# Kernel tuning notes

Hardware: AMD Instinct MI355X
Metric: run time of the kernel (lower is better)

Reference implementation:

```python
import jax, jax.numpy as jnp
import numpy as np

PI = float(np.pi)


def _cgs(node_feats, node_centre, nbr_idx, graph_w,
         mean_rho, mean_theta, prec_rho, prec_theta, conv_w, use_graph_weights):
    # node_feats: [B,N,C]; node_centre: [B,N,2]; nbr_idx: [B,N,K] (within-sample node ids)
    # graph_w: [B*N*K, 1] or None; mean/prec: [1,R]; conv_w: [R, C, OUT//R]
    B, N, C = node_feats.shape
    K = nbr_idx.shape[-1]
    R = mean_rho.shape[-1]
    BN = B * N
    # flat neighbor index into B*N nodes (coords[1])
    flat_nbr = (jnp.arange(B, dtype=nbr_idx.dtype)[:, None, None] * N + nbr_idx).reshape(BN * K)
    src = jnp.repeat(jnp.arange(BN), K)
    centre = node_centre.reshape(BN, 2)
    d = centre[src] - centre[flat_nbr]                    # [E,2], node_intersect 'minus'
    rho = jnp.sqrt(d[:, 0] ** 2 + d[:, 1] ** 2)
    theta = jnp.arctan2(d[:, 0], d[:, 1])
    # gaussian mixture edge weights over R kernels
    w_rho = jnp.exp(-0.5 * (rho[:, None] - mean_rho) ** 2 / (1e-14 + prec_rho ** 2))
    first_angle = jnp.abs(theta[:, None] - mean_theta)
    second_angle = jnp.abs(2.0 * PI - first_angle)
    w_theta = jnp.exp(-0.5 * jnp.minimum(first_angle, second_angle) ** 2
                      / (1e-14 + prec_theta ** 2))
    w = w_rho * w_theta
    w = jnp.where(jnp.isnan(w), 0.0, w)
    w = w / jnp.sum(w, axis=1, keepdims=True)             # [E,R]
    if use_graph_weights:
        w = graph_w * w
    ew = w.reshape(BN, K, R)
    nj = node_feats.reshape(BN, C)[flat_nbr].reshape(BN, K, C)   # gather neighbors
    agg = jnp.einsum('ekr,ekc->erc', ew, nj).reshape(B, N, R, C)  # weighted bmm
    out = jnp.einsum('bnrc,rcd->bnrd', agg, conv_w).reshape(B, N, R * conv_w.shape[-1])
    return jax.nn.relu(out)


def setup_inputs() -> dict:
    key = jax.random.key(0)
    ks = jax.random.split(key, 16)
    B, N, K, C, R, OUT = 64, 100, 16, 1024, 8, 1024
    D = OUT // R
    return {
        "node_feats": jax.random.normal(ks[0], (B, N, C), jnp.float32),
        "node_centre": jax.random.uniform(ks[1], (B, N, 2), dtype=jnp.float32),
        "graph_w": jax.random.uniform(ks[2], (B * N * K, 1), dtype=jnp.float32),
        "nbr_idx": jax.random.randint(ks[3], (B, N, K), 0, N, dtype=jnp.int32),
        "mean_rho1": jax.random.uniform(ks[4], (1, R), dtype=jnp.float32),
        "mean_theta1": jax.random.uniform(ks[5], (1, R), dtype=jnp.float32, minval=-PI, maxval=PI),
        "prec_rho1": jax.random.uniform(ks[6], (1, R), dtype=jnp.float32),
        "prec_theta1": jax.random.uniform(ks[7], (1, R), dtype=jnp.float32),
        "conv_w1": jax.random.normal(ks[8], (R, C, D), jnp.float32) * 0.02,
        "mean_rho2": jax.random.uniform(ks[9], (1, R), dtype=jnp.float32),
        "mean_theta2": jax.random.uniform(ks[10], (1, R), dtype=jnp.float32, minval=-PI, maxval=PI),
        "prec_rho2": jax.random.uniform(ks[11], (1, R), dtype=jnp.float32),
        "prec_theta2": jax.random.uniform(ks[12], (1, R), dtype=jnp.float32),
        "conv_w2": jax.random.normal(ks[13], (R, OUT, D), jnp.float32) * 0.02,
    }


def reference(node_feats, node_centre, graph_w,
              mean_rho1, mean_theta1, prec_rho1, prec_theta1, conv_w1,
              mean_rho2, mean_theta2, prec_rho2, prec_theta2, conv_w2,
              nbr_idx):
    # NodeFeatLayer('cgs_sum^8') = Sequential(CgsNodeFeat(use_graph_weights=True),
    #                                          CgsNodeFeat(use_graph_weights=False))
    h = _cgs(node_feats, node_centre, nbr_idx, graph_w,
             mean_rho1, mean_theta1, prec_rho1, prec_theta1, conv_w1, True)
    h = _cgs(h, node_centre, nbr_idx, None,
             mean_rho2, mean_theta2, prec_rho2, prec_theta2, conv_w2, False)
    return h
```

## Files before the change

kernel.cpp:

```cpp
#include <hip/hip_runtime.h>
#include <hip/hip_bf16.h>
#include <math.h>

#define B_   64
#define N_   100
#define K_   16
#define C_   1024
#define R_   8
#define BN_  6400
#define E_   102400

typedef __attribute__((ext_vector_type(8))) short bf16x8;
typedef __attribute__((ext_vector_type(4))) float f32x4;

__device__ __forceinline__ float bf2f(ushort h) {
    union { uint32_t u; float f; } v; v.u = ((uint32_t)h) << 16; return v.f;
}
__device__ __forceinline__ ushort f2bf(float f) {
    union { float f; uint32_t u; } v; v.f = f;
    uint32_t r = v.u + 0x7FFFu + ((v.u >> 16) & 1u);
    return (ushort)(r >> 16);
}

__device__ __forceinline__ void gload_lds16(const void* g, void* l) {
    __builtin_amdgcn_global_load_lds(
        (const __attribute__((address_space(1))) void*)g,
        (__attribute__((address_space(3))) void*)l, 16, 0, 0);
}

__global__ __launch_bounds__(256) void edge_weights_kernel(
        const float* __restrict__ centre, const int* __restrict__ nbr_idx,
        const float* __restrict__ graph_w,
        const float* __restrict__ mr1, const float* __restrict__ mt1,
        const float* __restrict__ pr1, const float* __restrict__ pt1,
        const float* __restrict__ mr2, const float* __restrict__ mt2,
        const float* __restrict__ pr2, const float* __restrict__ pt2,
        float* __restrict__ w1, float* __restrict__ w2) {
    int e = blockIdx.x * blockDim.x + threadIdx.x;
    if (e >= E_) return;
    int n = e / K_;
    int b = n / N_;
    int fn = b * N_ + nbr_idx[e];
    float dx = centre[2*n]   - centre[2*fn];
    float dy = centre[2*n+1] - centre[2*fn+1];
    float rho   = sqrtf(dx*dx + dy*dy);
    float theta = atan2f(dx, dy);
    const float TWO_PI = 6.28318530717958647692f;
    {
        float w[R_]; float s = 0.f;
        #pragma unroll
        for (int r = 0; r < R_; ++r) {
            float dr = rho - mr1[r];
            float wr = expf(-0.5f * dr * dr / (1e-14f + pr1[r]*pr1[r]));
            float fa = fabsf(theta - mt1[r]);
            float mi = fminf(fa, fabsf(TWO_PI - fa));
            float wt = expf(-0.5f * mi * mi / (1e-14f + pt1[r]*pt1[r]));
            float ww = wr * wt;
            if (isnan(ww)) ww = 0.f;
            w[r] = ww; s += ww;
        }
        float gw = graph_w[e];
        float4 o0 = { gw*(w[0]/s), gw*(w[1]/s), gw*(w[2]/s), gw*(w[3]/s) };
        float4 o1 = { gw*(w[4]/s), gw*(w[5]/s), gw*(w[6]/s), gw*(w[7]/s) };
        *(float4*)&w1[e*R_]     = o0;
        *(float4*)&w1[e*R_ + 4] = o1;
    }
    {
        float w[R_]; float s = 0.f;
        #pragma unroll
        for (int r = 0; r < R_; ++r) {
            float dr = rho - mr2[r];
            float wr = expf(-0.5f * dr * dr / (1e-14f + pr2[r]*pr2[r]));
            float fa = fabsf(theta - mt2[r]);
            float mi = fminf(fa, fabsf(TWO_PI - fa));
            float wt = expf(-0.5f * mi * mi / (1e-14f + pt2[r]*pt2[r]));
            float ww = wr * wt;
            if (isnan(ww)) ww = 0.f;
            w[r] = ww; s += ww;
        }
        float4 o0 = { w[0]/s, w[1]/s, w[2]/s, w[3]/s };
        float4 o1 = { w[4]/s, w[5]/s, w[6]/s, w[7]/s };
        *(float4*)&w2[e*R_]     = o0;
        *(float4*)&w2[e*R_ + 4] = o1;
    }
}

__global__ __launch_bounds__(256) void cast_x_kernel(
        const float* __restrict__ X, ushort* __restrict__ Xb) {
    int i = (blockIdx.x * 256 + threadIdx.x) * 4;
    float4 v = *(const float4*)&X[i];
    ushort4 o; o.x = f2bf(v.x); o.y = f2bf(v.y); o.z = f2bf(v.z); o.w = f2bf(v.w);
    *(ushort4*)&Xb[i] = o;
}

__global__ __launch_bounds__(256) void wtrans_kernel(
        const float* __restrict__ W1, ushort* __restrict__ Wt1,
        const float* __restrict__ W2, ushort* __restrict__ Wt2) {
    __shared__ ushort T[64][138];
    const float* W = (blockIdx.z == 0) ? W1 : W2;
    ushort*    Wt = (blockIdx.z == 0) ? Wt1 : Wt2;
    int r  = blockIdx.y;
    int c0 = blockIdx.x * 64;
    int t  = threadIdx.x;
    int lane6 = t & 63;
    #pragma unroll
    for (int it = 0; it < 16; ++it) {
        int ch = (t >> 6) + 4 * it;
        int d  = lane6 * 2;
        const float* src = &W[(((size_t)r << 10) + c0 + ch) * 128 + d];
        float2 v = *(const float2*)src;
        T[ch][d]     = f2bf(v.x);
        T[ch][d + 1] = f2bf(v.y);
    }
    __syncthreads();
    #pragma unroll
    for (int it = 0; it < 32; ++it) {
        int d = (t >> 6) + 4 * it;
        Wt[(size_t)(r * 128 + d) * 1024 + c0 + lane6] = T[lane6][d];
    }
}

__global__ __launch_bounds__(256) void gemm_bf16_kernel(
        const ushort* __restrict__ Xb,
        const ushort* __restrict__ Wt,
        ushort* __restrict__ P) {
    __shared__ ushort As[2][128][32];
    __shared__ ushort Bs[2][128][32];
    int tile = blockIdx.x;
    int swz  = (tile & 7) * 50 + (tile >> 3);
    int m0 = (swz >> 3) * 128, n0 = (swz & 7) * 128;
    int t = threadIdx.x, wid = t >> 6, lane = t & 63;
    int wr = wid >> 1, wc = wid & 1;

    int srow  = lane >> 2;
    int sslot = (lane & 3) ^ ((lane >> 2) & 3) ^ (lane >> 4);
    int pslot = (lane >> 4) ^ (lane & 3) ^ ((lane >> 2) & 3);

    f32x4 acc[4][4];
    #pragma unroll
    for (int i = 0; i < 4; ++i)
        #pragma unroll
        for (int j = 0; j < 4; ++j) acc[i][j] = (f32x4)0.f;

    int arow = wr * 64 + (lane & 15);
    int brow = wc * 64 + (lane & 15);
    int rowblk0 = wid * 16, rowblk1 = (4 + wid) * 16;
    const ushort* agp = Xb + (size_t)(m0 + srow) * 1024 + sslot * 8;
    const ushort* bgp = Wt + (size_t)(n0 + srow) * 1024 + sslot * 8;

    gload_lds16(agp + (size_t)rowblk0 * 1024, &As[0][rowblk0][0]);
    gload_lds16(bgp + (size_t)rowblk0 * 1024, &Bs[0][rowblk0][0]);
    gload_lds16(agp + (size_t)rowblk1 * 1024, &As[0][rowblk1][0]);
    gload_lds16(bgp + (size_t)rowblk1 * 1024, &Bs[0][rowblk1][0]);
    __syncthreads();

    for (int ts = 0; ts < 32; ++ts) {
        int cur = ts & 1;
        if (ts < 31) {
            int c1 = (ts + 1) * 32;
            gload_lds16(agp + (size_t)rowblk0 * 1024 + c1, &As[cur ^ 1][rowblk0][0]);
            gload_lds16(bgp + (size_t)rowblk0 * 1024 + c1, &Bs[cur ^ 1][rowblk0][0]);
            gload_lds16(agp + (size_t)rowblk1 * 1024 + c1, &As[cur ^ 1][rowblk1][0]);
            gload_lds16(bgp + (size_t)rowblk1 * 1024 + c1, &Bs[cur ^ 1][rowblk1][0]);
        }
        bf16x8 af[4], bfr[4];
        #pragma unroll
        for (int mi = 0; mi < 4; ++mi)
            af[mi] = *(const bf16x8*)&As[cur][arow + mi * 16][pslot * 8];
        #pragma unroll
        for (int ni = 0; ni < 4; ++ni)
            bfr[ni] = *(const bf16x8*)&Bs[cur][brow + ni * 16][pslot * 8];
        #pragma unroll
        for (int mi = 0; mi < 4; ++mi)
            #pragma unroll
            for (int ni = 0; ni < 4; ++ni)
                acc[mi][ni] = __builtin_amdgcn_mfma_f32_16x16x32_bf16(
                    af[mi], bfr[ni], acc[mi][ni], 0, 0, 0);
        __syncthreads();
    }
    int col = lane & 15, rq = lane >> 4;
    #pragma unroll
    for (int mi = 0; mi < 4; ++mi) {
        int row = m0 + wr * 64 + mi * 16 + rq * 4;
        #pragma unroll
        for (int ni = 0; ni < 4; ++ni) {
            int cc = n0 + wc * 64 + ni * 16 + col;
            #pragma unroll
            for (int q = 0; q < 4; ++q)
                P[(size_t)(row + q) * 1024 + cc] = f2bf(acc[mi][ni][q]);
        }
    }
}

__global__ __launch_bounds__(256) void aggregate_kernel(
        const ushort* __restrict__ P, const float* __restrict__ w,
        const int* __restrict__ nbr_idx,
        ushort* __restrict__ outB, float* __restrict__ outF) {
    __shared__ float wv[2][K_][R_];
    __shared__ int fnbr[2][K_];
    int bid = blockIdx.x;
    int n0 = ((bid & 7) * 400 + (bid >> 3)) * 2;
    int t = threadIdx.x;
    {
        int node = t >> 7, rem = t & 127, k = rem >> 3, r = rem & 7;
        wv[node][k][r] = w[((size_t)(n0 + node) * K_ + k) * R_ + r];
    }
    if (t < 32) {
        int node = t >> 4, k = t & 15, nn = n0 + node;
        fnbr[node][k] = (nn / N_) * N_ + nbr_idx[nn * K_ + k];
    }
    __syncthreads();
    int node = t >> 7, jj = t & 127;
    int j0 = jj * 8;
    int r  = jj >> 4;
    float a[8] = {};
    #pragma unroll
    for (int k = 0; k < K_; ++k) {
        bf16x8 v = *(const bf16x8*)&P[(size_t)fnbr[node][k] * 1024 + j0];
        float wk = wv[node][k][r];
        #pragma unroll
        for (int q = 0; q < 8; ++q) a[q] += wk * bf2f((ushort)v[q]);
    }
    #pragma unroll
    for (int q = 0; q < 8; ++q) a[q] = fmaxf(a[q], 0.f);
    size_t base = (size_t)(n0 + node) * 1024 + j0;
    if (outB) {
        bf16x8 o;
        #pragma unroll
        for (int q = 0; q < 8; ++q) o[q] = (short)f2bf(a[q]);
        *(bf16x8*)&outB[base] = o;
    } else {
        float4 o0 = { a[0], a[1], a[2], a[3] };
        float4 o1 = { a[4], a[5], a[6], a[7] };
        *(float4*)&outF[base]     = o0;
        *(float4*)&outF[base + 4] = o1;
    }
}

extern "C" void kernel_launch(void* const* d_in, const int* in_sizes, int n_in,
                              void* d_out, int out_size, void* d_ws, size_t ws_size,
                              hipStream_t stream) {
    const float* node_feats = (const float*)d_in[0];
    const float* centre     = (const float*)d_in[1];
    const float* graph_w    = (const float*)d_in[2];
    const int*   nbr_idx    = (const int*)  d_in[3];
    const float* mr1 = (const float*)d_in[4];
    const float* mt1 = (const float*)d_in[5];
    const float* pr1 = (const float*)d_in[6];
    const float* pt1 = (const float*)d_in[7];
    const float* cw1 = (const float*)d_in[8];
    const float* mr2 = (const float*)d_in[9];
    const float* mt2 = (const float*)d_in[10];
    const float* pr2 = (const float*)d_in[11];
    const float* pt2 = (const float*)d_in[12];
    const float* cw2 = (const float*)d_in[13];

    char* ws = (char*)d_ws;
    float*  w1  = (float*)ws;                 ws += (size_t)E_ * R_ * 4;
    float*  w2  = (float*)ws;                 ws += (size_t)E_ * R_ * 4;
    ushort* Xb  = (ushort*)ws;                ws += (size_t)BN_ * 1024 * 2;
    ushort* W1t = (ushort*)ws;                ws += (size_t)1024 * 1024 * 2;
    ushort* W2t = (ushort*)ws;                ws += (size_t)1024 * 1024 * 2;
    ushort* hb  = (ushort*)ws;                ws += (size_t)BN_ * 1024 * 2;
    ushort* P   = (ushort*)ws;

    float* out = (float*)d_out;

    edge_weights_kernel<<<(E_ + 255) / 256, 256, 0, stream>>>(
        centre, nbr_idx, graph_w, mr1, mt1, pr1, pt1, mr2, mt2, pr2, pt2, w1, w2);
    cast_x_kernel<<<BN_ * 1024 / 4 / 256, 256, 0, stream>>>(node_feats, Xb);
    wtrans_kernel<<<dim3(16, 8, 2), 256, 0, stream>>>(cw1, W1t, cw2, W2t);

    gemm_bf16_kernel<<<400, 256, 0, stream>>>(Xb, W1t, P);
    aggregate_kernel<<<BN_ / 2, 256, 0, stream>>>(P, w1, nbr_idx, hb, nullptr);

    gemm_bf16_kernel<<<400, 256, 0, stream>>>(hb, W2t, P);
    aggregate_kernel<<<BN_ / 2, 256, 0, stream>>>(P, w2, nbr_idx, nullptr, out);
}
```

Before: 192.5 us.

## Fuse per-sample GEMM with neighbor aggregation through LDS-resident projection tile

Replaces the separate GEMM and aggregation kernels with one kernel. Each block computes the projection for one sample (100 rows, padded to 112) and one 128-column chunk, which corresponds to one radial kernel r. The bf16 result is kept in swizzled LDS and the neighbor-weighted sum is done from there, so the intermediate P no longer round-trips through global memory. Edge weights are stored r-major so each block reads a contiguous slice of weights. The cost is 12.5% wasted MFMA rows from padding, heavier LDS use that lowers occupancy, and a narrower 7x2 tile per wave.

```diff
diff --git a/kernel.cpp b/kernel.cpp
--- a/kernel.cpp
+++ b/kernel.cpp
@@ -60,10 +60,8 @@
             w[r] = ww; s += ww;
         }
         float gw = graph_w[e];
-        float4 o0 = { gw*(w[0]/s), gw*(w[1]/s), gw*(w[2]/s), gw*(w[3]/s) };
-        float4 o1 = { gw*(w[4]/s), gw*(w[5]/s), gw*(w[6]/s), gw*(w[7]/s) };
-        *(float4*)&w1[e*R_]     = o0;
-        *(float4*)&w1[e*R_ + 4] = o1;
+        #pragma unroll
+        for (int r = 0; r < R_; ++r) w1[(size_t)r * E_ + e] = gw * (w[r] / s);
     }
     {
         float w[R_]; float s = 0.f;
@@ -78,10 +76,8 @@
             if (isnan(ww)) ww = 0.f;
             w[r] = ww; s += ww;
         }
-        float4 o0 = { w[0]/s, w[1]/s, w[2]/s, w[3]/s };
-        float4 o1 = { w[4]/s, w[5]/s, w[6]/s, w[7]/s };
-        *(float4*)&w2[e*R_]     = o0;
-        *(float4*)&w2[e*R_ + 4] = o1;
+        #pragma unroll
+        for (int r = 0; r < R_; ++r) w2[(size_t)r * E_ + e] = w[r] / s;
     }
 }
 
@@ -107,8 +103,7 @@
     for (int it = 0; it < 16; ++it) {
         int ch = (t >> 6) + 4 * it;
         int d  = lane6 * 2;
-        const float* src = &W[(((size_t)r << 10) + c0 + ch) * 128 + d];
-        float2 v = *(const float2*)src;
+        float2 v = *(const float2*)&W[(((size_t)r << 10) + c0 + ch) * 128 + d];
         T[ch][d]     = f2bf(v.x);
         T[ch][d + 1] = f2bf(v.y);
     }
@@ -120,120 +115,120 @@
     }
 }
 
-__global__ __launch_bounds__(256) void gemm_bf16_kernel(
+__global__ __launch_bounds__(256) void fused_gemm_agg_kernel(
         const ushort* __restrict__ Xb,
         const ushort* __restrict__ Wt,
-        ushort* __restrict__ P) {
-    __shared__ ushort As[2][128][32];
-    __shared__ ushort Bs[2][128][32];
-    int tile = blockIdx.x;
-    int swz  = (tile & 7) * 50 + (tile >> 3);
-    int m0 = (swz >> 3) * 128, n0 = (swz & 7) * 128;
+        const float* __restrict__ wR,
+        const int*   __restrict__ nbr,
+        ushort* __restrict__ outB,
+        float*  __restrict__ outF) {
+    __shared__ ushort Asb[2][112][32];
+    __shared__ ushort Bsb[2][128][32];
+    __shared__ ushort P_lds[100][128];
+    __shared__ float  w_lds[1600];
+    __shared__ int    f_lds[1600];
+
+    int bid = blockIdx.x;
+    int swz = (bid & 7) * 64 + (bid >> 3);
+    int sample = swz >> 3, cb = swz & 7;
     int t = threadIdx.x, wid = t >> 6, lane = t & 63;
-    int wr = wid >> 1, wc = wid & 1;
 
     int srow  = lane >> 2;
     int sslot = (lane & 3) ^ ((lane >> 2) & 3) ^ (lane >> 4);
     int pslot = (lane >> 4) ^ (lane & 3) ^ ((lane >> 2) & 3);
 
-    f32x4 acc[4][4];
-    #pragma unroll
-    for (int i = 0; i < 4; ++i)
-        #pragma unroll
-        for (int j = 0; j < 4; ++j) acc[i][j] = (f32x4)0.f;
-
-    int arow = wr * 64 + (lane & 15);
-    int brow = wc * 64 + (lane & 15);
-    int rowblk0 = wid * 16, rowblk1 = (4 + wid) * 16;
-    const ushort* agp = Xb + (size_t)(m0 + srow) * 1024 + sslot * 8;
-    const ushort* bgp = Wt + (size_t)(n0 + srow) * 1024 + sslot * 8;
-
-    gload_lds16(agp + (size_t)rowblk0 * 1024, &As[0][rowblk0][0]);
-    gload_lds16(bgp + (size_t)rowblk0 * 1024, &Bs[0][rowblk0][0]);
-    gload_lds16(agp + (size_t)rowblk1 * 1024, &As[0][rowblk1][0]);
-    gload_lds16(bgp + (size_t)rowblk1 * 1024, &Bs[0][rowblk1][0]);
+    const ushort* agp = Xb + (size_t)(sample * 100 + srow) * 1024 + sslot * 8;
+    const ushort* bgp = Wt + (size_t)(cb * 128 + srow) * 1024 + sslot * 8;
+
+    f32x4 acc[7][2];
+    #pragma unroll
+    for (int i = 0; i < 7; ++i) { acc[i][0] = (f32x4)0.f; acc[i][1] = (f32x4)0.f; }
+
+    #pragma unroll
+    for (int q = 0; q < 2; ++q) {
+        int ch = wid + 4 * q;
+        if (ch < 7) gload_lds16(agp + (size_t)ch * 16 * 1024, &Asb[0][ch * 16][0]);
+        gload_lds16(bgp + (size_t)ch * 16 * 1024, &Bsb[0][ch * 16][0]);
+    }
     __syncthreads();
 
     for (int ts = 0; ts < 32; ++ts) {
         int cur = ts & 1;
         if (ts < 31) {
             int c1 = (ts + 1) * 32;
-            gload_lds16(agp + (size_t)rowblk0 * 1024 + c1, &As[cur ^ 1][rowblk0][0]);
-            gload_lds16(bgp + (size_t)rowblk0 * 1024 + c1, &Bs[cur ^ 1][rowblk0][0]);
-            gload_lds16(agp + (size_t)rowblk1 * 1024 + c1, &As[cur ^ 1][rowblk1][0]);
-            gload_lds16(bgp + (size_t)rowblk1 * 1024 + c1, &Bs[cur ^ 1][rowblk1][0]);
-        }
-        bf16x8 af[4], bfr[4];
-        #pragma unroll
-        for (int mi = 0; mi < 4; ++mi)
-            af[mi] = *(const bf16x8*)&As[cur][arow + mi * 16][pslot * 8];
-        #pragma unroll
-        for (int ni = 0; ni < 4; ++ni)
-            bfr[ni] = *(const bf16x8*)&Bs[cur][brow + ni * 16][pslot * 8];
-        #pragma unroll
-        for (int mi = 0; mi < 4; ++mi)
             #pragma unroll
-            for (int ni = 0; ni < 4; ++ni)
+            for (int q = 0; q < 2; ++q) {
+                int ch = wid + 4 * q;
+                if (ch < 7) gload_lds16(agp + (size_t)ch * 16 * 1024 + c1,
+                                        &Asb[cur ^ 1][ch * 16][0]);
+                gload_lds16(bgp + (size_t)ch * 16 * 1024 + c1,
+                            &Bsb[cur ^ 1][ch * 16][0]);
+            }
+        }
+        bf16x8 af[7], bfr[2];
+        #pragma unroll
+        for (int mi = 0; mi < 7; ++mi)
+            af[mi] = *(const bf16x8*)&Asb[cur][mi * 16 + (lane & 15)][pslot * 8];
+        #pragma unroll
+        for (int ni = 0; ni < 2; ++ni)
+            bfr[ni] = *(const bf16x8*)&Bsb[cur][wid * 32 + ni * 16 + (lane & 15)][pslot * 8];
+        #pragma unroll
+        for (int mi = 0; mi < 7; ++mi)
+            #pragma unroll
+            for (int ni = 0; ni < 2; ++ni)
                 acc[mi][ni] = __builtin_amdgcn_mfma_f32_16x16x32_bf16(
                     af[mi], bfr[ni], acc[mi][ni], 0, 0, 0);
         __syncthreads();
     }
-    int col = lane & 15, rq = lane >> 4;
-    #pragma unroll
-    for (int mi = 0; mi < 4; ++mi) {
-        int row = m0 + wr * 64 + mi * 16 + rq * 4;
-        #pragma unroll
-        for (int ni = 0; ni < 4; ++ni) {
-            int cc = n0 + wc * 64 + ni * 16 + col;
+
+    #pragma unroll
+    for (int mi = 0; mi < 7; ++mi) {
+        #pragma unroll
+        for (int ni = 0; ni < 2; ++ni) {
+            int colb = wid * 32 + ni * 16 + (lane & 15);
             #pragma unroll
-            for (int q = 0; q < 4; ++q)
-                P[(size_t)(row + q) * 1024 + cc] = f2bf(acc[mi][ni][q]);
-        }
-    }
-}
-
-__global__ __launch_bounds__(256) void aggregate_kernel(
-        const ushort* __restrict__ P, const float* __restrict__ w,
-        const int* __restrict__ nbr_idx,
-        ushort* __restrict__ outB, float* __restrict__ outF) {
-    __shared__ float wv[2][K_][R_];
-    __shared__ int fnbr[2][K_];
-    int bid = blockIdx.x;
-    int n0 = ((bid & 7) * 400 + (bid >> 3)) * 2;
-    int t = threadIdx.x;
+            for (int q = 0; q < 4; ++q) {
+                int row = mi * 16 + (lane >> 4) * 4 + q;
+                if (row < 100) {
+                    int phys = colb ^ (((row >> 2) & 3) << 4);
+                    P_lds[row][phys] = f2bf(acc[mi][ni][q]);
+                }
+            }
+        }
+    }
     {
-        int node = t >> 7, rem = t & 127, k = rem >> 3, r = rem & 7;
-        wv[node][k][r] = w[((size_t)(n0 + node) * K_ + k) * R_ + r];
-    }
-    if (t < 32) {
-        int node = t >> 4, k = t & 15, nn = n0 + node;
-        fnbr[node][k] = (nn / N_) * N_ + nbr_idx[nn * K_ + k];
+        const float* wsrc = wR + (size_t)cb * E_ + (size_t)sample * 1600;
+        const int*   nsrc = nbr + (size_t)sample * 1600;
+        for (int i = t; i < 1600; i += 256) {
+            w_lds[i] = wsrc[i];
+            f_lds[i] = nsrc[i];
+        }
     }
     __syncthreads();
-    int node = t >> 7, jj = t & 127;
-    int j0 = jj * 8;
-    int r  = jj >> 4;
-    float a[8] = {};
-    #pragma unroll
-    for (int k = 0; k < K_; ++k) {
-        bf16x8 v = *(const bf16x8*)&P[(size_t)fnbr[node][k] * 1024 + j0];
-        float wk = wv[node][k][r];
-        #pragma unroll
-        for (int q = 0; q < 8; ++q) a[q] += wk * bf2f((ushort)v[q]);
-    }
-    #pragma unroll
-    for (int q = 0; q < 8; ++q) a[q] = fmaxf(a[q], 0.f);
-    size_t base = (size_t)(n0 + node) * 1024 + j0;
-    if (outB) {
-        bf16x8 o;
-        #pragma unroll
-        for (int q = 0; q < 8; ++q) o[q] = (short)f2bf(a[q]);
-        *(bf16x8*)&outB[base] = o;
-    } else {
-        float4 o0 = { a[0], a[1], a[2], a[3] };
-        float4 o1 = { a[4], a[5], a[6], a[7] };
-        *(float4*)&outF[base]     = o0;
-        *(float4*)&outF[base + 4] = o1;
+
+    int p = lane;
+    int nb = wid;
+    for (int i = 0; i < 25; ++i) {
+        int n = nb + 4 * i;
+        float a0 = 0.f, a1 = 0.f;
+        #pragma unroll
+        for (int k = 0; k < 16; ++k) {
+            int row  = f_lds[n * 16 + k];
+            float wk = w_lds[n * 16 + k];
+            ushort2 v = *(const ushort2*)&P_lds[row][(2 * p) ^ (((row >> 2) & 3) << 4)];
+            a0 += wk * bf2f(v.x);
+            a1 += wk * bf2f(v.y);
+        }
+        a0 = fmaxf(a0, 0.f);
+        a1 = fmaxf(a1, 0.f);
+        size_t base = (size_t)(sample * 100 + n) * 1024 + cb * 128 + 2 * p;
+        if (outB) {
+            ushort2 o; o.x = f2bf(a0); o.y = f2bf(a1);
+            *(ushort2*)&outB[base] = o;
+        } else {
+            float2 o; o.x = a0; o.y = a1;
+            *(float2*)&outF[base] = o;
+        }
     }
 }
 
@@ -256,13 +251,12 @@
     const float* cw2 = (const float*)d_in[13];
 
     char* ws = (char*)d_ws;
-    float*  w1  = (float*)ws;                 ws += (size_t)E_ * R_ * 4;
-    float*  w2  = (float*)ws;                 ws += (size_t)E_ * R_ * 4;
-    ushort* Xb  = (ushort*)ws;                ws += (size_t)BN_ * 1024 * 2;
-    ushort* W1t = (ushort*)ws;                ws += (size_t)1024 * 1024 * 2;
-    ushort* W2t = (ushort*)ws;                ws += (size_t)1024 * 1024 * 2;
-    ushort* hb  = (ushort*)ws;                ws += (size_t)BN_ * 1024 * 2;
-    ushort* P   = (ushort*)ws;
+    ushort* Xb  = (ushort*)ws;  ws += (size_t)BN_ * 1024 * 2;
+    ushort* W1t = (ushort*)ws;  ws += (size_t)1024 * 1024 * 2;
+    ushort* W2t = (ushort*)ws;  ws += (size_t)1024 * 1024 * 2;
+    ushort* hb  = (ushort*)ws;  ws += (size_t)BN_ * 1024 * 2;
+    float*  w1  = (float*)ws;   ws += (size_t)R_ * E_ * 4;
+    float*  w2  = (float*)ws;
 
     float* out = (float*)d_out;
 
@@ -271,9 +265,6 @@
     cast_x_kernel<<<BN_ * 1024 / 4 / 256, 256, 0, stream>>>(node_feats, Xb);
     wtrans_kernel<<<dim3(16, 8, 2), 256, 0, stream>>>(cw1, W1t, cw2, W2t);
 
-    gemm_bf16_kernel<<<400, 256, 0, stream>>>(Xb, W1t, P);
-    aggregate_kernel<<<BN_ / 2, 256, 0, stream>>>(P, w1, nbr_idx, hb, nullptr);
-
-    gemm_bf16_kernel<<<400, 256, 0, stream>>>(hb, W2t, P);
-    aggregate_kernel<<<BN_ / 2, 256, 0, stream>>>(P, w2, nbr_idx, nullptr, out);
-}
+    fused_gemm_agg_kernel<<<512, 256, 0, stream>>>(Xb, W1t, w1, nbr_idx, hb, nullptr);
+    fused_gemm_agg_kernel<<<512, 256, 0, stream>>>(hb, W2t, w2, nbr_idx, nullptr, out);
+}
```

After: 197.4 us. 2.5% more time.
